# Kernel tuning notes

Hardware: AMD Instinct MI355X
Metric: run time of the kernel (lower is better)

Reference implementation:

```python
import jax, jax.numpy as jnp
import numpy as np

# Model dims (Mamba-130M style)
BATCH, SEQ = 2, 1024
D_MODEL = 768
D_INNER = 1536          # 2 * d_model
DT_RANK = 48            # ceil(d_model / 16)
N_STATE = 16
D_CONV = 4
N_LAYER = 2
VOCAB = 50304           # 50257 padded to multiple of 64


def rms_norm(x, eps=1e-6):
    return x * jax.lax.rsqrt(jnp.mean(x * x, axis=-1, keepdims=True) + eps)


def setup_inputs():
    key = jax.random.key(0)
    ks = jax.random.split(key, 10)
    s = 3 ** 0.5 * D_MODEL ** -0.5
    si = 3 ** 0.5 * D_INNER ** -0.5
    # dt_proj bias init (inverse-softplus of dt in [1e-3, 1e-1]) as in init_weights
    u = jax.random.uniform(ks[6], (N_LAYER, D_INNER))
    dt = jnp.exp(u * (np.log(0.1) - np.log(0.001)) + np.log(0.001))
    dt = jnp.clip(dt, 1e-4)
    dt_proj_b = dt + jnp.log(-jnp.expm1(-dt))
    A_log = jnp.tile(jnp.log(jnp.arange(1, N_STATE + 1, dtype=jnp.float32)), (N_LAYER, D_INNER, 1))
    return {
        "tokens": jax.random.randint(ks[0], (BATCH, SEQ), 0, VOCAB),
        "wte": jax.random.normal(ks[1], (VOCAB, D_MODEL), dtype=jnp.float32) * 0.02,
        "in_proj_w": jax.random.uniform(ks[2], (N_LAYER, 2 * D_INNER, D_MODEL), minval=-s, maxval=s),
        "conv_w": jax.random.normal(ks[3], (N_LAYER, D_INNER, 1, D_CONV)) * 0.2,
        "conv_b": jnp.zeros((N_LAYER, D_INNER)),
        "x_proj_w": jax.random.uniform(ks[4], (N_LAYER, DT_RANK + 2 * N_STATE, D_INNER), minval=-si, maxval=si),
        "dt_proj_w": jax.random.uniform(ks[5], (N_LAYER, D_INNER, DT_RANK), minval=-DT_RANK ** -0.5, maxval=DT_RANK ** -0.5),
        "dt_proj_b": dt_proj_b,
        "out_proj_w": jax.random.normal(ks[7], (N_LAYER, D_MODEL, D_INNER)) * si * 0.1,
        "A_log": A_log,
        "D": jnp.ones((N_LAYER, D_INNER)),
        "lm_head_w": jax.random.normal(ks[8], (VOCAB, D_MODEL)) * 0.001,
    }


def _scan_combine(e1, e2):
    a1, b1 = e1
    a2, b2 = e2
    return (a1 * a2, a2 * b1 + b2)


def selective_scan(x, dt, A, Bs, Cs, Dp):
    # x, dt: (B,L,Di); A: (Di,N); Bs, Cs: (B,L,N); Dp: (Di,)
    dA = jnp.exp(dt[..., None] * A)                       # (B,L,Di,N)
    dBx = dt[..., None] * Bs[:, :, None, :] * x[..., None]  # (B,L,Di,N)
    _, h = jax.lax.associative_scan(_scan_combine, (dA, dBx), axis=1)
    y = jnp.einsum('bldn,bln->bld', h, Cs)
    return y + Dp * x


def _mixer(h, in_w, cw, cb, xp_w, dtp_w, dtp_b, out_w, A_log, Dp):
    xz = h @ in_w.T                                      # (B,L,2*Di)
    x, z = jnp.split(xz, 2, axis=-1)
    xc = jnp.transpose(x, (0, 2, 1))                     # (B,Di,L)
    xc = jax.lax.conv_general_dilated(
        xc, cw, window_strides=(1,), padding=[(D_CONV - 1, 0)],
        feature_group_count=D_INNER,
        dimension_numbers=('NCH', 'OIH', 'NCH')) + cb[None, :, None]
    x = jax.nn.silu(jnp.transpose(xc, (0, 2, 1)))        # (B,L,Di)
    x_dbl = x @ xp_w.T                                   # (B,L,dt_rank+2N)
    dt, Bs, Cs = jnp.split(x_dbl, [DT_RANK, DT_RANK + N_STATE], axis=-1)
    dt = jax.nn.softplus(dt @ dtp_w.T + dtp_b)
    A = -jnp.exp(A_log)
    y = selective_scan(x, dt, A, Bs, Cs, Dp)
    return (y * jax.nn.silu(z)) @ out_w.T


def reference(tokens, wte, in_proj_w, conv_w, conv_b, x_proj_w, dt_proj_w,
              dt_proj_b, out_proj_w, A_log, D, lm_head_w):
    x = wte[tokens]                                      # (B,L,D)
    for i in range(in_proj_w.shape[0]):
        x = x + _mixer(rms_norm(x), in_proj_w[i], conv_w[i], conv_b[i],
                       x_proj_w[i], dt_proj_w[i], dt_proj_b[i],
                       out_proj_w[i], A_log[i], D[i])
    x = rms_norm(x)
    return x @ lm_head_w.T                               # (B,L,VOCAB)
```

## Files before the change

### kernel.cpp

```cpp
#include <hip/hip_runtime.h>
#include <hip/hip_bf16.h>

#define BATCH 2
#define SEQ 1024
#define DMODEL 768
#define DINNER 1536
#define DTRANK 48
#define NSTATE 16
#define NLAYER 2
#define VOCAB 50304
#define NTOK (BATCH * SEQ)

typedef __attribute__((ext_vector_type(8))) short short8;
typedef __attribute__((ext_vector_type(4))) float f32x4;

__device__ __forceinline__ unsigned short f2bf(float f) {
    union { float f; unsigned u; } v; v.f = f;
    unsigned r = v.u + 0x7fffu + ((v.u >> 16) & 1u);
    return (unsigned short)(r >> 16);
}

__global__ __launch_bounds__(256) void cvt_bf16_kernel(const float* __restrict__ in,
                                                       unsigned short* __restrict__ out,
                                                       int n8) {
    int i = blockIdx.x * 256 + threadIdx.x;
    if (i >= n8) return;
    const float4* p = (const float4*)in + 2 * (size_t)i;
    float4 a = p[0], b = p[1];
    union { unsigned short us[8]; uint4 v; } o;
    o.us[0] = f2bf(a.x); o.us[1] = f2bf(a.y); o.us[2] = f2bf(a.z); o.us[3] = f2bf(a.w);
    o.us[4] = f2bf(b.x); o.us[5] = f2bf(b.y); o.us[6] = f2bf(b.z); o.us[7] = f2bf(b.w);
    ((uint4*)out)[i] = o.v;
}

template <int EPI>
__global__ __launch_bounds__(256) void gemm_bf16(const unsigned short* __restrict__ A, int lda,
                                                 const unsigned short* __restrict__ B, int ldb,
                                                 float* __restrict__ C, int ldc,
                                                 int K, int mtiles) {
    const int nwg = gridDim.x;
    const int bid = blockIdx.x;
    const int q = nwg >> 3, r = nwg & 7;
    const int xcd = bid & 7, loc = bid >> 3;
    const int wgid = (xcd < r ? xcd * (q + 1) : r * (q + 1) + (xcd - r) * q) + loc;
    const int m0 = (wgid % mtiles) * 128;
    const int n0 = (wgid / mtiles) * 128;

    __shared__ unsigned short As[128 * 32];
    __shared__ unsigned short Bs[128 * 32];
    const int tid = threadIdx.x;
    const int lane = tid & 63;
    const int wave = tid >> 6;
    const int wr = (wave >> 1) * 64;
    const int wc = (wave & 1) * 64;

    f32x4 acc[4][4] = {};

    for (int k0 = 0; k0 < K; k0 += 32) {
        __syncthreads();
        #pragma unroll
        for (int j = 0; j < 2; ++j) {
            int c = j * 256 + tid;
            int row = c >> 2;
            int kc = (c & 3) * 8;
            __builtin_amdgcn_global_load_lds(
                (const __attribute__((address_space(1))) unsigned int*)(A + (size_t)(m0 + row) * lda + k0 + kc),
                (__attribute__((address_space(3))) unsigned int*)(As + c * 8), 16, 0, 0);
            __builtin_amdgcn_global_load_lds(
                (const __attribute__((address_space(1))) unsigned int*)(B + (size_t)(n0 + row) * ldb + k0 + kc),
                (__attribute__((address_space(3))) unsigned int*)(Bs + c * 8), 16, 0, 0);
        }
        __syncthreads();

        short8 a[4], b[4];
        #pragma unroll
        for (int i = 0; i < 4; ++i)
            a[i] = *(const short8*)(As + (wr + i * 16 + (lane & 15)) * 32 + (lane >> 4) * 8);
        #pragma unroll
        for (int i = 0; i < 4; ++i)
            b[i] = *(const short8*)(Bs + (wc + i * 16 + (lane & 15)) * 32 + (lane >> 4) * 8);
        #pragma unroll
        for (int i = 0; i < 4; ++i)
            #pragma unroll
            for (int j = 0; j < 4; ++j)
                acc[i][j] = __builtin_amdgcn_mfma_f32_16x16x32_bf16(a[i], b[j], acc[i][j], 0, 0, 0);
    }

    const int row_base = m0 + wr + (lane >> 4) * 4;
    const int col_base = n0 + wc + (lane & 15);
    #pragma unroll
    for (int i = 0; i < 4; ++i)
        #pragma unroll
        for (int j = 0; j < 4; ++j)
            #pragma unroll
            for (int q2 = 0; q2 < 4; ++q2) {
                size_t idx = (size_t)(row_base + i * 16 + q2) * ldc + col_base + j * 16;
                if (EPI == 0) C[idx] = acc[i][j][q2];
                else          C[idx] += acc[i][j][q2];
            }
}

__global__ __launch_bounds__(256) void embed_kernel(const int* __restrict__ tokens,
                                                    const float* __restrict__ wte,
                                                    float* __restrict__ x) {
    int gid = blockIdx.x * 256 + threadIdx.x;
    int t = gid / (DMODEL / 4);
    int c = gid % (DMODEL / 4);
    if (t >= NTOK) return;
    int tok = tokens[t];
    ((float4*)x)[t * (DMODEL / 4) + c] = ((const float4*)wte)[(size_t)tok * (DMODEL / 4) + c];
}

__global__ __launch_bounds__(256) void rmsnorm_bf16_kernel(const float* __restrict__ in,
                                                           unsigned short* __restrict__ out) {
    int row = blockIdx.x;
    int tid = threadIdx.x;
    const float* r = in + row * DMODEL;
    float v0 = r[tid], v1 = r[tid + 256], v2 = r[tid + 512];
    float s = v0 * v0 + v1 * v1 + v2 * v2;
    #pragma unroll
    for (int off = 32; off > 0; off >>= 1) s += __shfl_down(s, off);
    __shared__ float red[4];
    int wid = tid >> 6, lane = tid & 63;
    if (lane == 0) red[wid] = s;
    __syncthreads();
    if (tid == 0) {
        float tot = red[0] + red[1] + red[2] + red[3];
        red[0] = 1.0f / sqrtf(tot / (float)DMODEL + 1e-6f);
    }
    __syncthreads();
    float sc = red[0];
    unsigned short* o = out + row * DMODEL;
    o[tid] = f2bf(v0 * sc); o[tid + 256] = f2bf(v1 * sc); o[tid + 512] = f2bf(v2 * sc);
}

template <int EPI>
__global__ __launch_bounds__(256) void gemm_tn(const float* __restrict__ A, int lda,
                                               const float* __restrict__ B, int ldb,
                                               float* __restrict__ C, int ldc,
                                               int M, int N, int K,
                                               const float* __restrict__ bias) {
    __shared__ float As[16][68];
    __shared__ float Bs[16][68];
    const int tid = threadIdx.x;
    const int m0 = blockIdx.y * 64;
    const int n0 = blockIdx.x * 64;
    const int lr = tid >> 2;
    const int lq = (tid & 3) * 4;
    const int tm = (tid & 15) * 4;
    const int tn = (tid >> 4) * 4;
    float acc[4][4] = {};

    for (int k0 = 0; k0 < K; k0 += 16) {
        float4 av = *(const float4*)(A + (m0 + lr) * lda + k0 + lq);
        float4 bv = make_float4(0.f, 0.f, 0.f, 0.f);
        if (n0 + lr < N) bv = *(const float4*)(B + (n0 + lr) * ldb + k0 + lq);
        __syncthreads();
        As[lq + 0][lr] = av.x; As[lq + 1][lr] = av.y; As[lq + 2][lr] = av.z; As[lq + 3][lr] = av.w;
        Bs[lq + 0][lr] = bv.x; Bs[lq + 1][lr] = bv.y; Bs[lq + 2][lr] = bv.z; Bs[lq + 3][lr] = bv.w;
        __syncthreads();
        #pragma unroll
        for (int kk = 0; kk < 16; ++kk) {
            float4 a = *(const float4*)&As[kk][tm];
            float4 b = *(const float4*)&Bs[kk][tn];
            const float* ap = (const float*)&a;
            const float* bp = (const float*)&b;
            #pragma unroll
            for (int i = 0; i < 4; ++i)
                #pragma unroll
                for (int j = 0; j < 4; ++j)
                    acc[i][j] = fmaf(ap[i], bp[j], acc[i][j]);
        }
    }

    #pragma unroll
    for (int i = 0; i < 4; ++i) {
        int m = m0 + tm + i;
        #pragma unroll
        for (int j = 0; j < 4; ++j) {
            int n = n0 + tn + j;
            if (n >= N) continue;
            float v = acc[i][j];
            if (EPI == 0) {
                C[m * ldc + n] = v;
            } else {
                v += bias[n];
                C[m * ldc + n] = (v > 20.f) ? v : log1pf(expf(v));
            }
        }
    }
}

__global__ __launch_bounds__(256) void conv_silu_kernel(const float* __restrict__ xz,
                                                        const float* __restrict__ cw,
                                                        const float* __restrict__ cb,
                                                        float* __restrict__ xs) {
    int gid = blockIdx.x * 256 + threadIdx.x;
    int d = gid % DINNER;
    int t = gid / DINNER;
    if (t >= NTOK) return;
    int l = t & (SEQ - 1);
    int tb = t - l;
    float4 w = ((const float4*)cw)[d];
    const float* wp = (const float*)&w;
    float acc = cb[d];
    #pragma unroll
    for (int k = 0; k < 4; ++k) {
        int lk = l - 3 + k;
        float v = (lk >= 0) ? xz[(tb + lk) * (2 * DINNER) + d] : 0.f;
        acc = fmaf(wp[k], v, acc);
    }
    xs[t * DINNER + d] = acc / (1.f + expf(-acc));
}

__global__ __launch_bounds__(256) void transpose2_kernel(const float* __restrict__ dtb,
                                                         const float* __restrict__ xs,
                                                         float* __restrict__ dt_t,
                                                         float* __restrict__ xs_t) {
    __shared__ float t0[32][33];
    __shared__ float t1[32][33];
    const int tid = threadIdx.x;
    const int tx = tid & 31, ty = tid >> 5;
    const int tbase = blockIdx.x * 32;
    const int dbase = blockIdx.y * 32;
    #pragma unroll
    for (int i = 0; i < 4; ++i) {
        int t = tbase + ty + i * 8;
        t0[ty + i * 8][tx] = dtb[(size_t)t * DINNER + dbase + tx];
        t1[ty + i * 8][tx] = xs[(size_t)t * DINNER + dbase + tx];
    }
    __syncthreads();
    const int b = tbase >> 10;
    const int l0 = tbase & (SEQ - 1);
    #pragma unroll
    for (int i = 0; i < 4; ++i) {
        int d = dbase + ty + i * 8;
        size_t o = (size_t)(b * DINNER + d) * SEQ + l0 + tx;
        dt_t[o] = t0[tx][ty + i * 8];
        xs_t[o] = t1[tx][ty + i * 8];
    }
}

__global__ __launch_bounds__(256) void scan2_kernel(const float* __restrict__ dt_t,
                                                    const float* __restrict__ x_t,
                                                    const float* __restrict__ xdbl,
                                                    const float* __restrict__ A_log,
                                                    const float* __restrict__ Dp,
                                                    float* __restrict__ y_t) {
    const int bd = blockIdx.x;
    const int d = bd % DINNER;
    const int b = bd / DINNER;
    const int tid = threadIdx.x;
    const int c = tid >> 4;
    const int n = tid & 15;

    const float* dtp = dt_t + (size_t)bd * SEQ + c * 64;
    const float* xp  = x_t  + (size_t)bd * SEQ + c * 64;
    const float* xd  = xdbl + (size_t)(b * SEQ + c * 64) * 80;
    const float A = -expf(A_log[d * NSTATE + n]);

    float a = 1.f, h = 0.f;
    #pragma unroll 4
    for (int qq = 0; qq < 16; ++qq) {
        float4 dq = ((const float4*)dtp)[qq];
        float4 xq = ((const float4*)xp)[qq];
        const float* dv = (const float*)&dq;
        const float* xv = (const float*)&xq;
        #pragma unroll
        for (int j = 0; j < 4; ++j) {
            int l = qq * 4 + j;
            float Bv = xd[l * 80 + DTRANK + n];
            float dA = expf(dv[j] * A);
            a *= dA;
            h = fmaf(h, dA, dv[j] * Bv * xv[j]);
        }
    }

    __shared__ float sa[16][16];
    __shared__ float sb[16][16];
    sa[c][n] = a; sb[c][n] = h;
    __syncthreads();
    if (tid < 16) {
        float hrun = 0.f;
        #pragma unroll
        for (int cc = 0; cc < 16; ++cc) {
            float av = sa[cc][tid];
            float bv = sb[cc][tid];
            sa[cc][tid] = hrun;
            hrun = fmaf(av, hrun, bv);
        }
    }
    __syncthreads();

    float hh = sa[c][n];
    const float Dv = Dp[d];
    float* yo = y_t + (size_t)bd * SEQ + c * 64;
    #pragma unroll 4
    for (int qq = 0; qq < 16; ++qq) {
        float4 dq = ((const float4*)dtp)[qq];
        float4 xq = ((const float4*)xp)[qq];
        const float* dv = (const float*)&dq;
        const float* xv = (const float*)&xq;
        #pragma unroll
        for (int j = 0; j < 4; ++j) {
            int l = qq * 4 + j;
            float Bv = xd[l * 80 + DTRANK + n];
            float Cv = xd[l * 80 + DTRANK + NSTATE + n];
            float dA = expf(dv[j] * A);
            hh = fmaf(hh, dA, dv[j] * Bv * xv[j]);
            float p = hh * Cv;
            p += __shfl_xor(p, 1, 16);
            p += __shfl_xor(p, 2, 16);
            p += __shfl_xor(p, 4, 16);
            p += __shfl_xor(p, 8, 16);
            if (n == 0) yo[l] = fmaf(Dv, xv[j], p);
        }
    }
}

__global__ __launch_bounds__(256) void gate_tr_kernel(const float* __restrict__ y_t,
                                                      const float* __restrict__ xz,
                                                      unsigned short* __restrict__ g) {
    __shared__ float ty_[32][33];
    const int tid = threadIdx.x;
    const int tx = tid & 31, ty = tid >> 5;
    const int tbase = blockIdx.x * 32;
    const int dbase = blockIdx.y * 32;
    const int b = tbase >> 10;
    const int l0 = tbase & (SEQ - 1);
    #pragma unroll
    for (int i = 0; i < 4; ++i) {
        int d = dbase + ty + i * 8;
        ty_[ty + i * 8][tx] = y_t[(size_t)(b * DINNER + d) * SEQ + l0 + tx];
    }
    __syncthreads();
    #pragma unroll
    for (int i = 0; i < 4; ++i) {
        int t = tbase + ty + i * 8;
        int d = dbase + tx;
        float z = xz[(size_t)t * (2 * DINNER) + DINNER + d];
        float yv = ty_[tx][ty + i * 8];
        float gv = yv * z / (1.f + expf(-z));
        g[(size_t)t * DINNER + d] = f2bf(gv);
    }
}

extern "C" void kernel_launch(void* const* d_in, const int* in_sizes, int n_in,
                              void* d_out, int out_size, void* d_ws, size_t ws_size,
                              hipStream_t stream) {
    const int*   tokens     = (const int*)d_in[0];
    const float* wte        = (const float*)d_in[1];
    const float* in_proj_w  = (const float*)d_in[2];
    const float* conv_w     = (const float*)d_in[3];
    const float* conv_b     = (const float*)d_in[4];
    const float* x_proj_w   = (const float*)d_in[5];
    const float* dt_proj_w  = (const float*)d_in[6];
    const float* dt_proj_b  = (const float*)d_in[7];
    const float* out_proj_w = (const float*)d_in[8];
    const float* A_log      = (const float*)d_in[9];
    const float* Dparam     = (const float*)d_in[10];
    const float* lm_head_w  = (const float*)d_in[11];
    float* out = (float*)d_out;

    float* ws   = (float*)d_ws;
    float* x    = ws;
    float* xz   = x    + NTOK * DMODEL;
    float* xs   = xz   + NTOK * 2 * DINNER;
    float* xdbl = xs   + NTOK * DINNER;
    float* dtb  = xdbl + NTOK * 80;
    float* dt_t = dtb  + NTOK * DINNER;
    float* xs_t = dt_t + NTOK * DINNER;
    float* y_t  = xs_t + NTOK * DINNER;
    unsigned short* xnb   = (unsigned short*)(y_t + NTOK * DINNER);
    unsigned short* gb    = xnb   + NTOK * DMODEL;
    unsigned short* inwb  = gb    + NTOK * DINNER;
    unsigned short* outwb = inwb  + 2 * 2 * DINNER * DMODEL;
    unsigned short* lmwb  = outwb + 2 * DMODEL * DINNER;

    {
        int n8 = 2 * 2 * DINNER * DMODEL / 8;
        cvt_bf16_kernel<<<(n8 + 255) / 256, 256, 0, stream>>>(in_proj_w, inwb, n8);
        n8 = 2 * DMODEL * DINNER / 8;
        cvt_bf16_kernel<<<(n8 + 255) / 256, 256, 0, stream>>>(out_proj_w, outwb, n8);
        n8 = VOCAB * DMODEL / 8;
        cvt_bf16_kernel<<<(n8 + 255) / 256, 256, 0, stream>>>(lm_head_w, lmwb, n8);
    }

    embed_kernel<<<NTOK * (DMODEL / 4) / 256, 256, 0, stream>>>(tokens, wte, x);

    for (int i = 0; i < NLAYER; ++i) {
        const unsigned short* inw = inwb + (size_t)i * 2 * DINNER * DMODEL;
        const float* cw   = conv_w     + (size_t)i * DINNER * 4;
        const float* cb   = conv_b     + (size_t)i * DINNER;
        const float* xpw  = x_proj_w   + (size_t)i * (DTRANK + 2 * NSTATE) * DINNER;
        const float* dtpw = dt_proj_w  + (size_t)i * DINNER * DTRANK;
        const float* dtpb = dt_proj_b  + (size_t)i * DINNER;
        const unsigned short* outw = outwb + (size_t)i * DMODEL * DINNER;
        const float* alog = A_log      + (size_t)i * DINNER * NSTATE;
        const float* dpar = Dparam     + (size_t)i * DINNER;

        rmsnorm_bf16_kernel<<<NTOK, 256, 0, stream>>>(x, xnb);
        gemm_bf16<0><<<(NTOK / 128) * (2 * DINNER / 128), 256, 0, stream>>>(
            xnb, DMODEL, inw, DMODEL, xz, 2 * DINNER, DMODEL, NTOK / 128);
        conv_silu_kernel<<<NTOK * DINNER / 256, 256, 0, stream>>>(xz, cw, cb, xs);
        gemm_tn<0><<<dim3(2, NTOK / 64), 256, 0, stream>>>(
            xs, DINNER, xpw, DINNER, xdbl, 80, NTOK, 80, DINNER, nullptr);
        gemm_tn<1><<<dim3(DINNER / 64, NTOK / 64), 256, 0, stream>>>(
            xdbl, 80, dtpw, DTRANK, dtb, DINNER, NTOK, DINNER, DTRANK, dtpb);
        transpose2_kernel<<<dim3(NTOK / 32, DINNER / 32), 256, 0, stream>>>(dtb, xs, dt_t, xs_t);
        scan2_kernel<<<BATCH * DINNER, 256, 0, stream>>>(dt_t, xs_t, xdbl, alog, dpar, y_t);
        gate_tr_kernel<<<dim3(NTOK / 32, DINNER / 32), 256, 0, stream>>>(y_t, xz, gb);
        gemm_bf16<2><<<(NTOK / 128) * (DMODEL / 128), 256, 0, stream>>>(
            gb, DINNER, outw, DINNER, x, DMODEL, DINNER, NTOK / 128);
    }

    rmsnorm_bf16_kernel<<<NTOK, 256, 0, stream>>>(x, xnb);
    gemm_bf16<0><<<(NTOK / 128) * (VOCAB / 128), 256, 0, stream>>>(
        xnb, DMODEL, lmwb, DMODEL, out, VOCAB, DMODEL, NTOK / 128);
}
```

Baseline: 1.379 ms.

## Fold x_proj dt-slice into dt_proj weight and run projections on bf16 MFMA

Precomputes a combined DINNER×DINNER weight W = dt_proj_w · x_proj_w[:48] on device, so the dt path becomes a single bf16 MFMA GEMM from xs, with softplus+bias fused into the epilogue. The B/C projection is moved to a split-K fp32 partial-plus-reduce pair, and the out_proj GEMM uses a new 64x64-tile MFMA kernel to give more workgroups. This removes the slow fp32 SIMT gemm_tn kernels but raises dt-path FLOPs (K=1536 instead of 48) and adds bf16 rounding of xs and the folded weight.

```diff
diff --git a/kernel.cpp b/kernel.cpp
--- a/kernel.cpp
+++ b/kernel.cpp
@@ -33,7 +33,6 @@
     ((uint4*)out)[i] = o.v;
 }
 
-template <int EPI>
 __global__ __launch_bounds__(256) void gemm_bf16(const unsigned short* __restrict__ A, int lda,
                                                  const unsigned short* __restrict__ B, int ldb,
                                                  float* __restrict__ C, int ldc,
@@ -95,8 +94,80 @@
             #pragma unroll
             for (int q2 = 0; q2 < 4; ++q2) {
                 size_t idx = (size_t)(row_base + i * 16 + q2) * ldc + col_base + j * 16;
-                if (EPI == 0) C[idx] = acc[i][j][q2];
-                else          C[idx] += acc[i][j][q2];
+                C[idx] = acc[i][j][q2];
+            }
+}
+
+template <int EPI>
+__global__ __launch_bounds__(256) void gemm64(const unsigned short* __restrict__ A, int lda,
+                                              const unsigned short* __restrict__ B, int ldb,
+                                              void* __restrict__ Cp, int ldc,
+                                              int K, int mtiles,
+                                              const float* __restrict__ bias) {
+    const int nwg = gridDim.x;
+    const int bid = blockIdx.x;
+    const int q = nwg >> 3, r = nwg & 7;
+    const int xcd = bid & 7, loc = bid >> 3;
+    const int wgid = (xcd < r ? xcd * (q + 1) : r * (q + 1) + (xcd - r) * q) + loc;
+    const int m0 = (wgid % mtiles) * 64;
+    const int n0 = (wgid / mtiles) * 64;
+
+    __shared__ unsigned short As[64 * 32];
+    __shared__ unsigned short Bs[64 * 32];
+    const int tid = threadIdx.x;
+    const int lane = tid & 63;
+    const int wave = tid >> 6;
+    const int wr = (wave >> 1) * 32;
+    const int wc = (wave & 1) * 32;
+    const int srow = tid >> 2;
+    const int skc = (tid & 3) * 8;
+
+    f32x4 acc[2][2] = {};
+
+    for (int k0 = 0; k0 < K; k0 += 32) {
+        __syncthreads();
+        __builtin_amdgcn_global_load_lds(
+            (const __attribute__((address_space(1))) unsigned int*)(A + (size_t)(m0 + srow) * lda + k0 + skc),
+            (__attribute__((address_space(3))) unsigned int*)(As + tid * 8), 16, 0, 0);
+        __builtin_amdgcn_global_load_lds(
+            (const __attribute__((address_space(1))) unsigned int*)(B + (size_t)(n0 + srow) * ldb + k0 + skc),
+            (__attribute__((address_space(3))) unsigned int*)(Bs + tid * 8), 16, 0, 0);
+        __syncthreads();
+
+        short8 a[2], b[2];
+        #pragma unroll
+        for (int i = 0; i < 2; ++i)
+            a[i] = *(const short8*)(As + (wr + i * 16 + (lane & 15)) * 32 + (lane >> 4) * 8);
+        #pragma unroll
+        for (int i = 0; i < 2; ++i)
+            b[i] = *(const short8*)(Bs + (wc + i * 16 + (lane & 15)) * 32 + (lane >> 4) * 8);
+        #pragma unroll
+        for (int i = 0; i < 2; ++i)
+            #pragma unroll
+            for (int j = 0; j < 2; ++j)
+                acc[i][j] = __builtin_amdgcn_mfma_f32_16x16x32_bf16(a[i], b[j], acc[i][j], 0, 0, 0);
+    }
+
+    const int row_base = m0 + wr + (lane >> 4) * 4;
+    const int col_base = n0 + wc + (lane & 15);
+    #pragma unroll
+    for (int i = 0; i < 2; ++i)
+        #pragma unroll
+        for (int j = 0; j < 2; ++j)
+            #pragma unroll
+            for (int q2 = 0; q2 < 4; ++q2) {
+                int rowg = row_base + i * 16 + q2;
+                int colg = col_base + j * 16;
+                size_t idx = (size_t)rowg * ldc + colg;
+                float v = acc[i][j][q2];
+                if (EPI == 1) {
+                    v += bias[colg];
+                    ((float*)Cp)[idx] = (v > 20.f) ? v : log1pf(expf(v));
+                } else if (EPI == 2) {
+                    ((float*)Cp)[idx] += v;
+                } else {
+                    ((unsigned short*)Cp)[idx] = f2bf(v);
+                }
             }
 }
 
@@ -134,67 +205,11 @@
     o[tid] = f2bf(v0 * sc); o[tid + 256] = f2bf(v1 * sc); o[tid + 512] = f2bf(v2 * sc);
 }
 
-template <int EPI>
-__global__ __launch_bounds__(256) void gemm_tn(const float* __restrict__ A, int lda,
-                                               const float* __restrict__ B, int ldb,
-                                               float* __restrict__ C, int ldc,
-                                               int M, int N, int K,
-                                               const float* __restrict__ bias) {
-    __shared__ float As[16][68];
-    __shared__ float Bs[16][68];
-    const int tid = threadIdx.x;
-    const int m0 = blockIdx.y * 64;
-    const int n0 = blockIdx.x * 64;
-    const int lr = tid >> 2;
-    const int lq = (tid & 3) * 4;
-    const int tm = (tid & 15) * 4;
-    const int tn = (tid >> 4) * 4;
-    float acc[4][4] = {};
-
-    for (int k0 = 0; k0 < K; k0 += 16) {
-        float4 av = *(const float4*)(A + (m0 + lr) * lda + k0 + lq);
-        float4 bv = make_float4(0.f, 0.f, 0.f, 0.f);
-        if (n0 + lr < N) bv = *(const float4*)(B + (n0 + lr) * ldb + k0 + lq);
-        __syncthreads();
-        As[lq + 0][lr] = av.x; As[lq + 1][lr] = av.y; As[lq + 2][lr] = av.z; As[lq + 3][lr] = av.w;
-        Bs[lq + 0][lr] = bv.x; Bs[lq + 1][lr] = bv.y; Bs[lq + 2][lr] = bv.z; Bs[lq + 3][lr] = bv.w;
-        __syncthreads();
-        #pragma unroll
-        for (int kk = 0; kk < 16; ++kk) {
-            float4 a = *(const float4*)&As[kk][tm];
-            float4 b = *(const float4*)&Bs[kk][tn];
-            const float* ap = (const float*)&a;
-            const float* bp = (const float*)&b;
-            #pragma unroll
-            for (int i = 0; i < 4; ++i)
-                #pragma unroll
-                for (int j = 0; j < 4; ++j)
-                    acc[i][j] = fmaf(ap[i], bp[j], acc[i][j]);
-        }
-    }
-
-    #pragma unroll
-    for (int i = 0; i < 4; ++i) {
-        int m = m0 + tm + i;
-        #pragma unroll
-        for (int j = 0; j < 4; ++j) {
-            int n = n0 + tn + j;
-            if (n >= N) continue;
-            float v = acc[i][j];
-            if (EPI == 0) {
-                C[m * ldc + n] = v;
-            } else {
-                v += bias[n];
-                C[m * ldc + n] = (v > 20.f) ? v : log1pf(expf(v));
-            }
-        }
-    }
-}
-
 __global__ __launch_bounds__(256) void conv_silu_kernel(const float* __restrict__ xz,
                                                         const float* __restrict__ cw,
                                                         const float* __restrict__ cb,
-                                                        float* __restrict__ xs) {
+                                                        float* __restrict__ xs,
+                                                        unsigned short* __restrict__ xsb) {
     int gid = blockIdx.x * 256 + threadIdx.x;
     int d = gid % DINNER;
     int t = gid / DINNER;
@@ -210,7 +225,52 @@
         float v = (lk >= 0) ? xz[(tb + lk) * (2 * DINNER) + d] : 0.f;
         acc = fmaf(wp[k], v, acc);
     }
-    xs[t * DINNER + d] = acc / (1.f + expf(-acc));
+    float sv = acc / (1.f + expf(-acc));
+    xs[t * DINNER + d] = sv;
+    xsb[t * DINNER + d] = f2bf(sv);
+}
+
+__global__ __launch_bounds__(256) void prep_wdt_kernel(const float* __restrict__ dtp_w,
+                                                       const float* __restrict__ xp_w,
+                                                       unsigned short* __restrict__ dtpwb,
+                                                       unsigned short* __restrict__ xp48T) {
+    int gid = blockIdx.x * 256 + threadIdx.x;
+    int rr = gid >> 6, k = gid & 63;
+    dtpwb[gid] = (k < 48) ? f2bf(dtp_w[rr * 48 + k]) : (unsigned short)0;
+    xp48T[gid] = (k < 48) ? f2bf(xp_w[k * DINNER + rr]) : (unsigned short)0;
+}
+
+__global__ __launch_bounds__(256) void bc_partial_kernel(const float* __restrict__ xs,
+                                                         const float* __restrict__ bcw,
+                                                         float* __restrict__ part) {
+    const int kc = blockIdx.x;
+    const int mt = blockIdx.y;
+    const int j  = threadIdx.x & 31;
+    const int rg = threadIdx.x >> 5;
+    const float* brow = bcw + (size_t)j * DINNER + kc * 128;
+    #pragma unroll 1
+    for (int rr = 0; rr < 16; ++rr) {
+        int row = mt * 128 + rg * 16 + rr;
+        const float* arow = xs + (size_t)row * DINNER + kc * 128;
+        float acc = 0.f;
+        #pragma unroll
+        for (int qq = 0; qq < 32; ++qq) {
+            float4 av = ((const float4*)arow)[qq];
+            float4 bv = ((const float4*)brow)[qq];
+            acc = fmaf(av.x, bv.x, acc); acc = fmaf(av.y, bv.y, acc);
+            acc = fmaf(av.z, bv.z, acc); acc = fmaf(av.w, bv.w, acc);
+        }
+        part[((size_t)kc * NTOK + row) * 32 + j] = acc;
+    }
+}
+
+__global__ __launch_bounds__(256) void bc_reduce_kernel(const float* __restrict__ part,
+                                                        float* __restrict__ xbc) {
+    int gid = blockIdx.x * 256 + threadIdx.x;
+    float s = 0.f;
+    #pragma unroll
+    for (int kc = 0; kc < 12; ++kc) s += part[(size_t)kc * (NTOK * 32) + gid];
+    xbc[gid] = s;
 }
 
 __global__ __launch_bounds__(256) void transpose2_kernel(const float* __restrict__ dtb,
@@ -243,7 +303,7 @@
 
 __global__ __launch_bounds__(256) void scan2_kernel(const float* __restrict__ dt_t,
                                                     const float* __restrict__ x_t,
-                                                    const float* __restrict__ xdbl,
+                                                    const float* __restrict__ xbc,
                                                     const float* __restrict__ A_log,
                                                     const float* __restrict__ Dp,
                                                     float* __restrict__ y_t) {
@@ -256,7 +316,7 @@
 
     const float* dtp = dt_t + (size_t)bd * SEQ + c * 64;
     const float* xp  = x_t  + (size_t)bd * SEQ + c * 64;
-    const float* xd  = xdbl + (size_t)(b * SEQ + c * 64) * 80;
+    const float* xb  = xbc + (size_t)(b * SEQ + c * 64) * 32;
     const float A = -expf(A_log[d * NSTATE + n]);
 
     float a = 1.f, h = 0.f;
@@ -269,7 +329,7 @@
         #pragma unroll
         for (int j = 0; j < 4; ++j) {
             int l = qq * 4 + j;
-            float Bv = xd[l * 80 + DTRANK + n];
+            float Bv = xb[l * 32 + n];
             float dA = expf(dv[j] * A);
             a *= dA;
             h = fmaf(h, dA, dv[j] * Bv * xv[j]);
@@ -304,8 +364,8 @@
         #pragma unroll
         for (int j = 0; j < 4; ++j) {
             int l = qq * 4 + j;
-            float Bv = xd[l * 80 + DTRANK + n];
-            float Cv = xd[l * 80 + DTRANK + NSTATE + n];
+            float Bv = xb[l * 32 + n];
+            float Cv = xb[l * 32 + 16 + n];
             float dA = expf(dv[j] * A);
             hh = fmaf(hh, dA, dv[j] * Bv * xv[j]);
             float p = hh * Cv;
@@ -366,16 +426,21 @@
     float* x    = ws;
     float* xz   = x    + NTOK * DMODEL;
     float* xs   = xz   + NTOK * 2 * DINNER;
-    float* xdbl = xs   + NTOK * DINNER;
-    float* dtb  = xdbl + NTOK * 80;
+    float* dtb  = xs   + NTOK * DINNER;
     float* dt_t = dtb  + NTOK * DINNER;
     float* xs_t = dt_t + NTOK * DINNER;
-    float* y_t  = xs_t + NTOK * DINNER;
-    unsigned short* xnb   = (unsigned short*)(y_t + NTOK * DINNER);
-    unsigned short* gb    = xnb   + NTOK * DMODEL;
-    unsigned short* inwb  = gb    + NTOK * DINNER;
-    unsigned short* outwb = inwb  + 2 * 2 * DINNER * DMODEL;
-    unsigned short* lmwb  = outwb + 2 * DMODEL * DINNER;
+    float* xbc  = xs_t + NTOK * DINNER;
+    float* y_t    = dtb;
+    float* bcpart = dt_t;
+    unsigned short* xnb    = (unsigned short*)(xbc + NTOK * 32);
+    unsigned short* xsb    = xnb    + NTOK * DMODEL;
+    unsigned short* gb     = xsb    + NTOK * DINNER;
+    unsigned short* inwb   = gb     + NTOK * DINNER;
+    unsigned short* outwb  = inwb   + 2 * 2 * DINNER * DMODEL;
+    unsigned short* lmwb   = outwb  + 2 * DMODEL * DINNER;
+    unsigned short* dtpwb  = lmwb   + (size_t)VOCAB * DMODEL;
+    unsigned short* xp48Tb = dtpwb  + DINNER * 64;
+    unsigned short* Wdtb   = xp48Tb + DINNER * 64;
 
     {
         int n8 = 2 * 2 * DINNER * DMODEL / 8;
@@ -400,21 +465,24 @@
         const float* dpar = Dparam     + (size_t)i * DINNER;
 
         rmsnorm_bf16_kernel<<<NTOK, 256, 0, stream>>>(x, xnb);
-        gemm_bf16<0><<<(NTOK / 128) * (2 * DINNER / 128), 256, 0, stream>>>(
+        gemm_bf16<<<(NTOK / 128) * (2 * DINNER / 128), 256, 0, stream>>>(
             xnb, DMODEL, inw, DMODEL, xz, 2 * DINNER, DMODEL, NTOK / 128);
-        conv_silu_kernel<<<NTOK * DINNER / 256, 256, 0, stream>>>(xz, cw, cb, xs);
-        gemm_tn<0><<<dim3(2, NTOK / 64), 256, 0, stream>>>(
-            xs, DINNER, xpw, DINNER, xdbl, 80, NTOK, 80, DINNER, nullptr);
-        gemm_tn<1><<<dim3(DINNER / 64, NTOK / 64), 256, 0, stream>>>(
-            xdbl, 80, dtpw, DTRANK, dtb, DINNER, NTOK, DINNER, DTRANK, dtpb);
+        conv_silu_kernel<<<NTOK * DINNER / 256, 256, 0, stream>>>(xz, cw, cb, xs, xsb);
+        prep_wdt_kernel<<<DINNER * 64 / 256, 256, 0, stream>>>(dtpw, xpw, dtpwb, xp48Tb);
+        gemm64<3><<<(DINNER / 64) * (DINNER / 64), 256, 0, stream>>>(
+            dtpwb, 64, xp48Tb, 64, Wdtb, DINNER, 64, DINNER / 64, nullptr);
+        gemm64<1><<<(NTOK / 64) * (DINNER / 64), 256, 0, stream>>>(
+            xsb, DINNER, Wdtb, DINNER, dtb, DINNER, DINNER, NTOK / 64, dtpb);
+        bc_partial_kernel<<<dim3(12, 16), 256, 0, stream>>>(xs, xpw + 48 * DINNER, bcpart);
+        bc_reduce_kernel<<<NTOK * 32 / 256, 256, 0, stream>>>(bcpart, xbc);
         transpose2_kernel<<<dim3(NTOK / 32, DINNER / 32), 256, 0, stream>>>(dtb, xs, dt_t, xs_t);
-        scan2_kernel<<<BATCH * DINNER, 256, 0, stream>>>(dt_t, xs_t, xdbl, alog, dpar, y_t);
+        scan2_kernel<<<BATCH * DINNER, 256, 0, stream>>>(dt_t, xs_t, xbc, alog, dpar, y_t);
         gate_tr_kernel<<<dim3(NTOK / 32, DINNER / 32), 256, 0, stream>>>(y_t, xz, gb);
-        gemm_bf16<2><<<(NTOK / 128) * (DMODEL / 128), 256, 0, stream>>>(
-            gb, DINNER, outw, DINNER, x, DMODEL, DINNER, NTOK / 128);
+        gemm64<2><<<(NTOK / 64) * (DMODEL / 64), 256, 0, stream>>>(
+            gb, DINNER, outw, DINNER, x, DMODEL, DINNER, NTOK / 64, nullptr);
     }
 
     rmsnorm_bf16_kernel<<<NTOK, 256, 0, stream>>>(x, xnb);
-    gemm_bf16<0><<<(NTOK / 128) * (VOCAB / 128), 256, 0, stream>>>(
+    gemm_bf16<<<(NTOK / 128) * (VOCAB / 128), 256, 0, stream>>>(
         xnb, DMODEL, lmwb, DMODEL, out, VOCAB, DMODEL, NTOK / 128);
 }
```

Measured after the change: 1.319 ms. -4.4%, faster.
